# Kernel optimization log

Measured on AMD Instinct MI355X. Metric: run time of the kernel, lower is better.

Reference implementation:

```python
import jax, jax.numpy as jnp
import numpy as np

CHANNELS = 512
GROUPS = 32
EPS = 1e-6


def setup_inputs() -> dict:
    key = jax.random.key(0)
    ks = jax.random.split(key, 10)
    C = CHANNELS
    s = 1.0 / np.sqrt(C)
    return {
        "hidden_states": jax.random.normal(ks[0], (4, 64, 64, C), dtype=jnp.float32),
        "gn_scale": jnp.ones((C,), dtype=jnp.float32),
        "gn_bias": jnp.zeros((C,), dtype=jnp.float32),
        "wq": jax.random.normal(ks[1], (C, C), dtype=jnp.float32) * s,
        "bq": jnp.zeros((C,), dtype=jnp.float32),
        "wk": jax.random.normal(ks[2], (C, C), dtype=jnp.float32) * s,
        "bk": jnp.zeros((C,), dtype=jnp.float32),
        "wv": jax.random.normal(ks[3], (C, C), dtype=jnp.float32) * s,
        "bv": jnp.zeros((C,), dtype=jnp.float32),
        "wo": jax.random.normal(ks[4], (C, C), dtype=jnp.float32) * s,
        "bo": jnp.zeros((C,), dtype=jnp.float32),
    }


def reference(hidden_states, gn_scale, gn_bias, wq, bq, wk, bk, wv, bv, wo, bo):
    B, H, W, C = hidden_states.shape
    residual = hidden_states
    L = H * W
    x = hidden_states.reshape(B, L, C)

    # GroupNorm: stats over (spatial, channels-within-group), per batch per group
    xg = x.reshape(B, L, GROUPS, C // GROUPS)
    mean = jnp.mean(xg, axis=(1, 3), keepdims=True)
    var = jnp.var(xg, axis=(1, 3), keepdims=True)
    xn = ((xg - mean) * jax.lax.rsqrt(var + EPS)).reshape(B, L, C)
    xn = xn * gn_scale + gn_bias

    # QKV projections (heads=1, head_dim=C)
    q = xn @ wq + bq
    k = xn @ wk + bk
    v = xn @ wv + bv

    scale = 1.0 / jnp.sqrt(jnp.asarray(C, dtype=q.dtype))
    scores = jnp.einsum('bld,bsd->bls', q, k) * scale  # [B, L, L]
    attn = jax.nn.softmax(scores, axis=-1)
    out = jnp.einsum('bls,bsd->bld', attn, v)

    out = out @ wo + bo
    return out.reshape(B, H, W, C) + residual
```

## Files before the change

kernel.cpp:

```cpp
#include <hip/hip_runtime.h>
#include <hip/hip_bf16.h>
#include <stdint.h>

#define BATCH 4
#define SEQ   4096
#define CH    512
#define NGRP  32
#define GEPS  1e-6f

typedef short  short8  __attribute__((ext_vector_type(8)));
typedef float  floatx4 __attribute__((ext_vector_type(4)));
typedef long   longx2  __attribute__((ext_vector_type(2)));

static __device__ __forceinline__ short bf16b(float f) {
    __hip_bfloat16 h = __float2bfloat16(f);
    return __builtin_bit_cast(short, h);
}
static __device__ __forceinline__ float bf2f(short s) {
    unsigned u = ((unsigned)(unsigned short)s) << 16;
    return __builtin_bit_cast(float, u);
}
static __device__ __forceinline__ char fp8b(float f) {
    int pk = __builtin_amdgcn_cvt_pk_fp8_f32(f, f, 0, false);
    return (char)(pk & 0xff);
}

static __device__ __forceinline__ void dma16(const void* g, void* l) {
    __builtin_amdgcn_global_load_lds(
        (const __attribute__((address_space(1))) unsigned int*)g,
        (__attribute__((address_space(3))) unsigned int*)l, 16, 0, 0);
}

static __device__ __forceinline__ float rowmax16(float x) {
    int xi = __builtin_bit_cast(int, x);
    x = fmaxf(x, __builtin_bit_cast(float, __builtin_amdgcn_update_dpp(xi, xi, 0x128, 0xf, 0xf, true)));
    xi = __builtin_bit_cast(int, x);
    x = fmaxf(x, __builtin_bit_cast(float, __builtin_amdgcn_update_dpp(xi, xi, 0x124, 0xf, 0xf, true)));
    xi = __builtin_bit_cast(int, x);
    x = fmaxf(x, __builtin_bit_cast(float, __builtin_amdgcn_update_dpp(xi, xi, 0x122, 0xf, 0xf, true)));
    xi = __builtin_bit_cast(int, x);
    x = fmaxf(x, __builtin_bit_cast(float, __builtin_amdgcn_update_dpp(xi, xi, 0x121, 0xf, 0xf, true)));
    return x;
}

__global__ __launch_bounds__(256) void gn_wt_kernel(const float* __restrict__ x,
                                                    float* __restrict__ statsraw,
                                                    const float* __restrict__ w0,
                                                    const float* __restrict__ w1,
                                                    const float* __restrict__ w2,
                                                    const float* __restrict__ w3,
                                                    short* __restrict__ wT) {
    __shared__ float a1[256], a2[256];
    __shared__ float trs[32][33];
    int blk = blockIdx.x;
    int t = threadIdx.x;
    if (blk < 256) {
        size_t row0 = (size_t)blk * 64;
        int qd = t & 127;
        int rh = t >> 7;
        const float* base = x + row0 * 512 + qd * 4;
        float s1 = 0.f, s2 = 0.f;
        #pragma unroll 4
        for (int i = 0; i < 32; ++i) {
            int r = rh + i * 2;
            float4 v = *reinterpret_cast<const float4*>(base + (size_t)r * 512);
            s1 += v.x + v.y + v.z + v.w;
            s2 += v.x * v.x + v.y * v.y + v.z * v.z + v.w * v.w;
        }
        a1[t] = s1; a2[t] = s2;
        __syncthreads();
        if (t < 32) {
            float u1 = 0.f, u2 = 0.f;
            #pragma unroll
            for (int e = 0; e < 4; ++e) {
                u1 += a1[t * 4 + e] + a1[128 + t * 4 + e];
                u2 += a2[t * 4 + e] + a2[128 + t * 4 + e];
            }
            int b = (int)(row0 >> 12);
            atomicAdd(&statsraw[(b * 32 + t) * 2],     u1);
            atomicAdd(&statsraw[(b * 32 + t) * 2 + 1], u2);
        }
    } else {
        int bz = (blk - 256) >> 8;
        int rem = (blk - 256) & 255;
        int n0 = (rem & 15) * 32, k0 = (rem >> 4) * 32;
        const float* w = (bz == 0) ? w0 : (bz == 1) ? w1 : (bz == 2) ? w2 : w3;
        short* out = wT + (size_t)bz * CH * CH;
        int tx = t & 31, ty = t >> 5;
        #pragma unroll
        for (int i = 0; i < 4; ++i) {
            int kk = ty + i * 8;
            trs[kk][tx] = w[(size_t)(k0 + kk) * CH + n0 + tx];
        }
        __syncthreads();
        #pragma unroll
        for (int i = 0; i < 4; ++i) {
            int nn = ty + i * 8;
            out[(size_t)(n0 + nn) * CH + k0 + tx] = bf16b(trs[tx][nn]);
        }
    }
}

__global__ __launch_bounds__(256) void gn_apply_kernel(const float* __restrict__ x,
                                                       const float* __restrict__ statsraw,
                                                       const float* __restrict__ gsc,
                                                       const float* __restrict__ gbs,
                                                       short* __restrict__ xn) {
    int i4 = blockIdx.x * 256 + threadIdx.x;
    int base = i4 * 4;
    int b = base >> 21;
    int c = base & 511;
    int sidx = (b * 32 + (c >> 4)) * 2;
    float s1 = statsraw[sidx], s2 = statsraw[sidx + 1];
    float mean = s1 * (1.f / 65536.f);
    float var  = s2 * (1.f / 65536.f) - mean * mean;
    float rstd = rsqrtf(var + GEPS);
    float4 xv = reinterpret_cast<const float4*>(x)[i4];
    float4 sv = *reinterpret_cast<const float4*>(gsc + c);
    float4 bv = *reinterpret_cast<const float4*>(gbs + c);
    union { short s[4]; uint2 u; } p;
    p.s[0] = bf16b((xv.x - mean) * rstd * sv.x + bv.x);
    p.s[1] = bf16b((xv.y - mean) * rstd * sv.y + bv.y);
    p.s[2] = bf16b((xv.z - mean) * rstd * sv.z + bv.z);
    p.s[3] = bf16b((xv.w - mean) * rstd * sv.w + bv.w);
    reinterpret_cast<uint2*>(xn)[i4] = p.u;
}

__global__ __launch_bounds__(256) void gemm_qkv_kernel(const short* __restrict__ A,
                                                       const short* __restrict__ wT,
                                                       const float* __restrict__ bq,
                                                       const float* __restrict__ bk,
                                                       const float* __restrict__ bv,
                                                       char* __restrict__ q8,
                                                       char* __restrict__ k8,
                                                       char* __restrict__ vT8) {
    __shared__ short As[128 * 64];
    __shared__ short Bs[128 * 64];
    __shared__ char  vls[128 * 144];
    int m0 = blockIdx.x * 128;
    int nblk = blockIdx.y;
    int which = nblk >> 2;
    int n0 = (nblk & 3) * 128;
    const short* BT = wT + (size_t)which * 512 * 512;
    const float* bias = (which == 0) ? bq : (which == 1) ? bk : bv;
    int t = threadIdx.x;
    int w = t >> 6, lane = t & 63;
    int wr = w >> 1, wc = w & 1;
    int l15 = lane & 15, l4 = lane >> 4;
    floatx4 acc[4][4];
    #pragma unroll
    for (int i = 0; i < 4; ++i)
        #pragma unroll
        for (int j = 0; j < 4; ++j) acc[i][j] = (floatx4){0.f, 0.f, 0.f, 0.f};

    for (int k0 = 0; k0 < 512; k0 += 64) {
        __syncthreads();
        #pragma unroll
        for (int i = 0; i < 4; ++i) {
            int c = i * 256 + t;
            int row = c >> 3, j = (c & 7) ^ (row & 7);
            dma16(&A[(size_t)(m0 + row) * 512 + k0 + j * 8], &As[(c & ~63) * 8]);
            dma16(&BT[(size_t)(n0 + row) * 512 + k0 + j * 8], &Bs[(c & ~63) * 8]);
        }
        __syncthreads();
        #pragma unroll
        for (int kk = 0; kk < 64; kk += 32) {
            short8 af[4], bf[4];
            #pragma unroll
            for (int i = 0; i < 4; ++i) {
                int row = wr * 64 + i * 16 + l15;
                int j = (kk >> 3) + l4;
                af[i] = *reinterpret_cast<const short8*>(&As[(row * 8 + (j ^ (l15 & 7))) * 8]);
            }
            #pragma unroll
            for (int j2 = 0; j2 < 4; ++j2) {
                int row = wc * 64 + j2 * 16 + l15;
                int j = (kk >> 3) + l4;
                bf[j2] = *reinterpret_cast<const short8*>(&Bs[(row * 8 + (j ^ (l15 & 7))) * 8]);
            }
            #pragma unroll
            for (int i = 0; i < 4; ++i)
                #pragma unroll
                for (int j2 = 0; j2 < 4; ++j2)
                    acc[i][j2] = __builtin_amdgcn_mfma_f32_16x16x32_bf16(af[i], bf[j2], acc[i][j2], 0, 0, 0);
        }
    }
    if (which == 0) {
        #pragma unroll
        for (int i = 0; i < 4; ++i)
            #pragma unroll
            for (int j = 0; j < 4; ++j)
                #pragma unroll
                for (int r = 0; r < 4; ++r) {
                    int rl = wr * 64 + i * 16 + l4 * 4 + r;
                    int cl = wc * 64 + j * 16 + l15;
                    vls[rl * 144 + cl] = fp8b(acc[i][j][r] + bias[n0 + cl]);
                }
        __syncthreads();
        #pragma unroll
        for (int p = 0; p < 4; ++p) {
            int slot = p * 256 + t;
            int c = slot >> 3, off = (slot & 7) * 16;
            uint4 v;
            __builtin_memcpy(&v, &vls[c * 144 + off], 16);
            *reinterpret_cast<uint4*>(&q8[(size_t)(m0 + c) * 512 + n0 + off]) = v;
        }
    } else if (which == 1) {
        #pragma unroll
        for (int i = 0; i < 4; ++i)
            #pragma unroll
            for (int j = 0; j < 4; ++j)
                #pragma unroll
                for (int r = 0; r < 4; ++r) {
                    int rl = wr * 64 + i * 16 + l4 * 4 + r;
                    int cl = wc * 64 + j * 16 + l15;
                    int sblk = rl >> 5, srow = rl & 15, hp = (rl >> 4) & 1;
                    int ch = (cl >> 3) ^ (srow & 7);
                    vls[sblk * 4096 + srow * 256 + ch * 16 + hp * 8 + (cl & 7)]
                        = fp8b(acc[i][j][r] + bias[n0 + cl]);
                }
        __syncthreads();
        int bb = m0 >> 12, sb0 = (m0 & 4095) >> 5;
        #pragma unroll
        for (int p = 0; p < 4; ++p) {
            int u = p * 256 + t;
            int sblk = u >> 8, srow = (u >> 4) & 15, ch = u & 15;
            uint4 v;
            __builtin_memcpy(&v, &vls[sblk * 4096 + srow * 256 + ((ch ^ (srow & 7)) * 16)], 16);
            char* dst = k8 + (size_t)bb * 2097152 + (size_t)(sb0 + sblk) * 16384
                      + srow * 1024 + n0 * 2 + ch * 16;
            *reinterpret_cast<uint4*>(dst) = v;
        }
    } else {
        __syncthreads();
        #pragma unroll
        for (int i = 0; i < 4; ++i)
            #pragma unroll
            for (int j = 0; j < 4; ++j)
                #pragma unroll
                for (int r = 0; r < 4; ++r) {
                    int rl = wr * 64 + i * 16 + l4 * 4 + r;
                    int rp = (rl & ~31) | (((rl & 15) << 1) | ((rl >> 4) & 1));
                    int cl = wc * 64 + j * 16 + l15;
                    vls[cl * 144 + rp] = fp8b(acc[i][j][r] + bias[n0 + cl]);
                }
        __syncthreads();
        int b = m0 >> 12, l0 = m0 & 4095;
        #pragma unroll
        for (int p = 0; p < 4; ++p) {
            int slot = p * 256 + t;
            int c = slot >> 3, off = (slot & 7) * 16;
            uint4 v;
            __builtin_memcpy(&v, &vls[c * 144 + off], 16);
            int dcol = n0 + c;
            int g = dcol >> 5, rr = dcol & 15, h = (dcol >> 4) & 1;
            int s = l0 + off;
            int sb = s >> 5, mb = (s & 31) >> 3;
            char* dst = vT8 + (size_t)b * 2097152 + (size_t)sb * 16384
                      + (size_t)((((g * 16 + rr) * 4 + mb) * 16) + h * 8);
            unsigned long long lo = ((unsigned long long)v.y << 32) | v.x;
            unsigned long long hi = ((unsigned long long)v.w << 32) | v.z;
            *reinterpret_cast<unsigned long long*>(dst)      = lo;
            *reinterpret_cast<unsigned long long*>(dst + 16) = hi;
        }
    }
}

__global__ __launch_bounds__(256) void gemm_bt_kernel(const short* __restrict__ Opart,
                                                      const float* __restrict__ ml,
                                                      const short* __restrict__ BT,
                                                      const float* __restrict__ bias,
                                                      float* __restrict__ outf,
                                                      const float* __restrict__ resid) {
    __shared__ short As[128 * 64];
    __shared__ short Bs[128 * 64];
    int m0 = blockIdx.x * 128, n0 = blockIdx.y * 128;
    int t = threadIdx.x;
    int w = t >> 6, lane = t & 63;
    int wr = w >> 1, wc = w & 1;
    int l15 = lane & 15, l4 = lane >> 4;
    const size_t PART = (size_t)BATCH * SEQ;
    floatx4 acc[4][4];
    #pragma unroll
    for (int i = 0; i < 4; ++i)
        #pragma unroll
        for (int j = 0; j < 4; ++j) acc[i][j] = (floatx4){0.f, 0.f, 0.f, 0.f};

    float e0h[4], e1h[4];
    #pragma unroll
    for (int i = 0; i < 4; ++i) {
        int rl = (i * 256 + t) >> 3;
        size_t rowg = (size_t)(m0 + rl);
        float mA = ml[rowg * 2],          lA = ml[rowg * 2 + 1];
        float mB = ml[(PART + rowg) * 2], lB = ml[(PART + rowg) * 2 + 1];
        float mm = fmaxf(mA, mB);
        float e0 = exp2f(mA - mm), e1 = exp2f(mB - mm);
        float inv = 1.f / (e0 * lA + e1 * lB);
        e0h[i] = e0 * inv; e1h[i] = e1 * inv;
    }

    for (int k0 = 0; k0 < 512; k0 += 64) {
        __syncthreads();
        #pragma unroll
        for (int i = 0; i < 4; ++i) {
            int c = i * 256 + t;
            int rl = c >> 3, j = (c & 7) ^ (rl & 7);
            size_t rowg = (size_t)(m0 + rl);
            const short* s0 = Opart + rowg * 512 + k0 + j * 8;
            const short* s1 = s0 + PART * 512;
            uint4 a0 = *reinterpret_cast<const uint4*>(s0);
            uint4 a1 = *reinterpret_cast<const uint4*>(s1);
            union { uint4 u; short s[8]; } ua, ub, uo;
            ua.u = a0; ub.u = a1;
            #pragma unroll
            for (int e = 0; e < 8; ++e)
                uo.s[e] = bf16b(bf2f(ua.s[e]) * e0h[i] + bf2f(ub.s[e]) * e1h[i]);
            *reinterpret_cast<uint4*>(&As[c * 8]) = uo.u;
            dma16(&BT[(size_t)(n0 + rl) * 512 + k0 + j * 8], &Bs[(c & ~63) * 8]);
        }
        __syncthreads();
        #pragma unroll
        for (int kk = 0; kk < 64; kk += 32) {
            short8 af[4], bf[4];
            #pragma unroll
            for (int i = 0; i < 4; ++i) {
                int row = wr * 64 + i * 16 + l15;
                int j = (kk >> 3) + l4;
                af[i] = *reinterpret_cast<const short8*>(&As[(row * 8 + (j ^ (l15 & 7))) * 8]);
            }
            #pragma unroll
            for (int j2 = 0; j2 < 4; ++j2) {
                int row = wc * 64 + j2 * 16 + l15;
                int j = (kk >> 3) + l4;
                bf[j2] = *reinterpret_cast<const short8*>(&Bs[(row * 8 + (j ^ (l15 & 7))) * 8]);
            }
            #pragma unroll
            for (int i = 0; i < 4; ++i)
                #pragma unroll
                for (int j2 = 0; j2 < 4; ++j2)
                    acc[i][j2] = __builtin_amdgcn_mfma_f32_16x16x32_bf16(af[i], bf[j2], acc[i][j2], 0, 0, 0);
        }
    }
    #pragma unroll
    for (int i = 0; i < 4; ++i)
        #pragma unroll
        for (int j = 0; j < 4; ++j)
            #pragma unroll
            for (int r = 0; r < 4; ++r) {
                int row = m0 + wr * 64 + i * 16 + l4 * 4 + r;
                int col = n0 + wc * 64 + j * 16 + l15;
                float vv = acc[i][j][r] + bias[col];
                outf[(size_t)row * 512 + col] = vv + resid[(size_t)row * 512 + col];
            }
}

__global__ __launch_bounds__(512, 1) void flash_kernel(const char* __restrict__ q8,
                                                       const char* __restrict__ k8,
                                                       const char* __restrict__ v8,
                                                       short* __restrict__ Opart,
                                                       float* __restrict__ ml) {
    __shared__ __align__(16) char smem[141312];
    int bx = blockIdx.x;
    int pb = bx & 7;
    int part = pb >> 2, b = pb & 3;
    int q0 = (bx >> 3) * 128;
    int t = threadIdx.x, w = t >> 6, lane = t & 63;
    int l15 = lane & 15, l4 = lane >> 4;
    const float c2 = 0.06375873735f;
    const float MARGIN = 7.2134752f;

    long qf[16];
    {
        const char* qrow = q8 + ((size_t)b * SEQ + q0 + w * 16 + l15) * 512;
        #pragma unroll
        for (int ks = 0; ks < 16; ++ks)
            qf[ks] = *reinterpret_cast<const long*>(qrow + ks * 32 + l4 * 8);
    }

    floatx4 acc[32];
    #pragma unroll
    for (int i = 0; i < 32; ++i) acc[i] = (floatx4){0.f, 0.f, 0.f, 0.f};
    floatx4 lacc = (floatx4){0.f, 0.f, 0.f, 0.f};
    float mused[4] = {-1e30f, -1e30f, -1e30f, -1e30f};

    const long ones = 0x3838383838383838L;

    const char* kbase = k8 + (size_t)b * SEQ * 512;
    const char* vbase = v8 + (size_t)b * 512 * SEQ;
    const int sb0 = part * 64;

    const int ksw = l15 & 7;
    const int vsw = (l15 >> 1) & 3;
    const char* kA_E = smem + ((l15 * 64 + (l4 ^ ksw)) << 4);
    const char* kA_O = smem + ((l15 * 64 + ((4 + l4) ^ ksw)) << 4);
    const char* vA   = smem + 65536 + ((l15 * 4 + (l4 ^ vsw)) << 4);
    char* Ps = smem + 131072 + w * 1280;

    int kSrc[4], vSrc[4];
    #pragma unroll
    for (int i = 0; i < 4; ++i) {
        int c = i * 512 + t;
        int tile = c >> 10, cw = c & 1023;
        kSrc[i] = tile * 16384 + (((cw & ~63) | ((cw & 63) ^ ((cw >> 6) & 7))) << 4);
        vSrc[i] = tile * 16384 + (((cw & ~3)  | ((cw & 3)  ^ ((cw >> 3) & 3))) << 4);
    }
    const int ldsD = (t & ~63) << 4;

    auto stage = [&](int sb, int buf) {
        const char* kt = kbase + (size_t)sb * 16384;
        const char* vt = vbase + (size_t)sb * 16384;
        char* Kd = smem + buf * 32768 + ldsD;
        char* Vd = smem + 65536 + buf * 32768 + ldsD;
        #pragma unroll
        for (int i = 0; i < 4; ++i) dma16(kt + kSrc[i], Kd + i * 8192);
        #pragma unroll
        for (int i = 0; i < 4; ++i) dma16(vt + vSrc[i], Vd + i * 8192);
    };

    stage(sb0, 0);
    __syncthreads();

    for (int it = 0; it < 32; ++it) {
        int cur = it & 1;
        int coff = cur << 15;
        if (it + 1 < 32) stage(sb0 + 2 * (it + 1), 1 - cur);

        floatx4 s00 = (floatx4){0.f, 0.f, 0.f, 0.f};
        floatx4 s01 = (floatx4){0.f, 0.f, 0.f, 0.f};
        floatx4 s10 = (floatx4){0.f, 0.f, 0.f, 0.f};
        floatx4 s11 = (floatx4){0.f, 0.f, 0.f, 0.f};
        #pragma unroll
        for (int j = 0; j < 8; ++j) {
            longx2 kE0 = *reinterpret_cast<const longx2*>(kA_E + coff + j * 128);
            longx2 kO0 = *reinterpret_cast<const longx2*>(kA_O + coff + j * 128);
            longx2 kE1 = *reinterpret_cast<const longx2*>(kA_E + coff + 16384 + j * 128);
            longx2 kO1 = *reinterpret_cast<const longx2*>(kA_O + coff + 16384 + j * 128);
            s00 = __builtin_amdgcn_mfma_f32_16x16x32_fp8_fp8(qf[2 * j],     kE0[0], s00, 0, 0, 0);
            s01 = __builtin_amdgcn_mfma_f32_16x16x32_fp8_fp8(qf[2 * j],     kE0[1], s01, 0, 0, 0);
            s10 = __builtin_amdgcn_mfma_f32_16x16x32_fp8_fp8(qf[2 * j],     kE1[0], s10, 0, 0, 0);
            s11 = __builtin_amdgcn_mfma_f32_16x16x32_fp8_fp8(qf[2 * j],     kE1[1], s11, 0, 0, 0);
            s00 = __builtin_amdgcn_mfma_f32_16x16x32_fp8_fp8(qf[2 * j + 1], kO0[0], s00, 0, 0, 0);
            s01 = __builtin_amdgcn_mfma_f32_16x16x32_fp8_fp8(qf[2 * j + 1], kO0[1], s01, 0, 0, 0);
            s10 = __builtin_amdgcn_mfma_f32_16x16x32_fp8_fp8(qf[2 * j + 1], kO1[0], s10, 0, 0, 0);
            s11 = __builtin_amdgcn_mfma_f32_16x16x32_fp8_fp8(qf[2 * j + 1], kO1[1], s11, 0, 0, 0);
        }

        float v00[4], v01[4], v10[4], v11[4], nm4[4];
        bool need = false;
        #pragma unroll
        for (int r = 0; r < 4; ++r) {
            v00[r] = s00[r] * c2; v01[r] = s01[r] * c2;
            v10[r] = s10[r] * c2; v11[r] = s11[r] * c2;
            nm4[r] = rowmax16(fmaxf(fmaxf(v00[r], v01[r]), fmaxf(v10[r], v11[r])));
            need |= (nm4[r] > mused[r] + MARGIN);
        }
        if (__ballot(need)) {
            #pragma unroll
            for (int r = 0; r < 4; ++r) {
                float nm = fmaxf(mused[r], nm4[r]);
                float al = exp2f(mused[r] - nm);
                lacc[r] *= al;
                #pragma unroll
                for (int i = 0; i < 32; ++i) acc[i][r] *= al;
                mused[r] = nm;
            }
        }
        #pragma unroll
        for (int r = 0; r < 4; ++r) {
            int pk0 = __builtin_amdgcn_cvt_pk_fp8_f32(exp2f(v00[r] - mused[r]),
                                                      exp2f(v01[r] - mused[r]), 0, false);
            int pk1 = __builtin_amdgcn_cvt_pk_fp8_f32(exp2f(v10[r] - mused[r]),
                                                      exp2f(v11[r] - mused[r]), 0, false);
            *reinterpret_cast<short*>(Ps + (l4 * 4 + r) * 40 + l15 * 2)       = (short)pk0;
            *reinterpret_cast<short*>(Ps + 640 + (l4 * 4 + r) * 40 + l15 * 2) = (short)pk1;
        }

        long pf0, pf1;
        __builtin_memcpy(&pf0, (const char*)__builtin_assume_aligned(Ps + l15 * 40 + l4 * 8, 8), 8);
        __builtin_memcpy(&pf1, (const char*)__builtin_assume_aligned(Ps + 640 + l15 * 40 + l4 * 8, 8), 8);
        lacc = __builtin_amdgcn_mfma_f32_16x16x32_fp8_fp8(pf0, ones, lacc, 0, 0, 0);
        lacc = __builtin_amdgcn_mfma_f32_16x16x32_fp8_fp8(pf1, ones, lacc, 0, 0, 0);
        #pragma unroll
        for (int g = 0; g < 16; ++g) {
            longx2 va = *reinterpret_cast<const longx2*>(vA + coff + g * 1024);
            acc[2 * g]     = __builtin_amdgcn_mfma_f32_16x16x32_fp8_fp8(pf0, va[0], acc[2 * g],     0, 0, 0);
            acc[2 * g + 1] = __builtin_amdgcn_mfma_f32_16x16x32_fp8_fp8(pf0, va[1], acc[2 * g + 1], 0, 0, 0);
        }
        #pragma unroll
        for (int g = 0; g < 16; ++g) {
            longx2 vb = *reinterpret_cast<const longx2*>(vA + coff + 16384 + g * 1024);
            acc[2 * g]     = __builtin_amdgcn_mfma_f32_16x16x32_fp8_fp8(pf1, vb[0], acc[2 * g],     0, 0, 0);
            acc[2 * g + 1] = __builtin_amdgcn_mfma_f32_16x16x32_fp8_fp8(pf1, vb[1], acc[2 * g + 1], 0, 0, 0);
        }

        __syncthreads();
    }

    short* obase = Opart + (((size_t)part * BATCH + b) * SEQ + q0 + w * 16) * 512;
    #pragma unroll
    for (int r = 0; r < 4; ++r) {
        #pragma unroll
        for (int tt = 0; tt < 32; ++tt)
            obase[(size_t)(l4 * 4 + r) * 512 + tt * 16 + l15] = bf16b(acc[tt][r]);
    }
    if (l15 == 0) {
        #pragma unroll
        for (int r = 0; r < 4; ++r) {
            size_t rowg = ((size_t)part * BATCH + b) * SEQ + q0 + w * 16 + l4 * 4 + r;
            ml[rowg * 2]     = mused[r];
            ml[rowg * 2 + 1] = lacc[r];
        }
    }
}

extern "C" void kernel_launch(void* const* d_in, const int* in_sizes, int n_in,
                              void* d_out, int out_size, void* d_ws, size_t ws_size,
                              hipStream_t stream) {
    const float* x   = (const float*)d_in[0];
    const float* gsc = (const float*)d_in[1];
    const float* gbs = (const float*)d_in[2];
    const float* wq  = (const float*)d_in[3];
    const float* bq  = (const float*)d_in[4];
    const float* wk  = (const float*)d_in[5];
    const float* bk  = (const float*)d_in[6];
    const float* wv  = (const float*)d_in[7];
    const float* bv  = (const float*)d_in[8];
    const float* wo  = (const float*)d_in[9];
    const float* bo  = (const float*)d_in[10];
    float* out = (float*)d_out;

    char* ws = (char*)d_ws;
    const size_t MB = 1ull << 20;
    short* xn    = (short*)ws;
    char*  q8    = (char*)(ws + 16 * MB);
    char*  k8    = (char*)(ws + 24 * MB);
    char*  vT8   = (char*)(ws + 32 * MB);
    short* Opart = (short*)(ws + 40 * MB);
    short* wT    = (short*)(ws + 72 * MB);
    float* stats = (float*)(ws + 74 * MB);
    float* ml    = (float*)(ws + 74 * MB + 65536);

    hipMemsetAsync(stats, 0, 256 * sizeof(float), stream);
    gn_wt_kernel<<<1280, 256, 0, stream>>>(x, stats, wq, wk, wv, wo, wT);
    gn_apply_kernel<<<8192, 256, 0, stream>>>(x, stats, gsc, gbs, xn);

    short* woT = wT + 786432;

    gemm_qkv_kernel<<<dim3(128, 12), 256, 0, stream>>>(xn, wT, bq, bk, bv, q8, k8, vT8);
    flash_kernel<<<256, 512, 0, stream>>>(q8, k8, vT8, Opart, ml);
    gemm_bt_kernel<<<dim3(128, 4), 256, 0, stream>>>(Opart, ml, woT, bo, out, x);
}
```

Measured before the change: 277.6 us.

## Process two 16-row query groups per wave in flash kernel with 4 waves

The flash attention block shrinks from 8 waves to 4, and each wave now handles two 16-row query groups. Each K/V fragment read from LDS therefore feeds two sets of MFMAs, which halves LDS read traffic per unit of compute and improves reuse. The cost is twice the accumulator registers per wave (64 floatx4 for O plus Q fragments). With one block per CU and 4 waves, occupancy and latency hiding drop, and register spilling is a risk.

New measurement: 836.3 us. 201% more time.

```diff
diff --git a/kernel.cpp b/kernel.cpp
--- a/kernel.cpp
+++ b/kernel.cpp
@@ -354,7 +354,7 @@
             }
 }
 
-__global__ __launch_bounds__(512, 1) void flash_kernel(const char* __restrict__ q8,
+__global__ __launch_bounds__(256, 1) void flash_kernel(const char* __restrict__ q8,
                                                        const char* __restrict__ k8,
                                                        const char* __restrict__ v8,
                                                        short* __restrict__ Opart,
@@ -369,19 +369,25 @@
     const float c2 = 0.06375873735f;
     const float MARGIN = 7.2134752f;
 
-    long qf[16];
-    {
-        const char* qrow = q8 + ((size_t)b * SEQ + q0 + w * 16 + l15) * 512;
+    long qf[2][16];
+    #pragma unroll
+    for (int qg = 0; qg < 2; ++qg) {
+        const char* qrow = q8 + ((size_t)b * SEQ + q0 + qg * 64 + w * 16 + l15) * 512;
         #pragma unroll
         for (int ks = 0; ks < 16; ++ks)
-            qf[ks] = *reinterpret_cast<const long*>(qrow + ks * 32 + l4 * 8);
-    }
-
-    floatx4 acc[32];
-    #pragma unroll
-    for (int i = 0; i < 32; ++i) acc[i] = (floatx4){0.f, 0.f, 0.f, 0.f};
-    floatx4 lacc = (floatx4){0.f, 0.f, 0.f, 0.f};
-    float mused[4] = {-1e30f, -1e30f, -1e30f, -1e30f};
+            qf[qg][ks] = *reinterpret_cast<const long*>(qrow + ks * 32 + l4 * 8);
+    }
+
+    floatx4 acc[2][32];
+    #pragma unroll
+    for (int qg = 0; qg < 2; ++qg)
+        #pragma unroll
+        for (int i = 0; i < 32; ++i) acc[qg][i] = (floatx4){0.f, 0.f, 0.f, 0.f};
+    floatx4 lacc[2];
+    lacc[0] = (floatx4){0.f, 0.f, 0.f, 0.f};
+    lacc[1] = (floatx4){0.f, 0.f, 0.f, 0.f};
+    float mused[2][4] = {{-1e30f, -1e30f, -1e30f, -1e30f},
+                         {-1e30f, -1e30f, -1e30f, -1e30f}};
 
     const long ones = 0x3838383838383838L;
 
@@ -394,12 +400,12 @@
     const char* kA_E = smem + ((l15 * 64 + (l4 ^ ksw)) << 4);
     const char* kA_O = smem + ((l15 * 64 + ((4 + l4) ^ ksw)) << 4);
     const char* vA   = smem + 65536 + ((l15 * 4 + (l4 ^ vsw)) << 4);
-    char* Ps = smem + 131072 + w * 1280;
-
-    int kSrc[4], vSrc[4];
-    #pragma unroll
-    for (int i = 0; i < 4; ++i) {
-        int c = i * 512 + t;
+    char* Ps = smem + 131072 + w * 2560;
+
+    int kSrc[8], vSrc[8];
+    #pragma unroll
+    for (int i = 0; i < 8; ++i) {
+        int c = i * 256 + t;
         int tile = c >> 10, cw = c & 1023;
         kSrc[i] = tile * 16384 + (((cw & ~63) | ((cw & 63) ^ ((cw >> 6) & 7))) << 4);
         vSrc[i] = tile * 16384 + (((cw & ~3)  | ((cw & 3)  ^ ((cw >> 3) & 3))) << 4);
@@ -412,9 +418,9 @@
         char* Kd = smem + buf * 32768 + ldsD;
         char* Vd = smem + 65536 + buf * 32768 + ldsD;
         #pragma unroll
-        for (int i = 0; i < 4; ++i) dma16(kt + kSrc[i], Kd + i * 8192);
-        #pragma unroll
-        for (int i = 0; i < 4; ++i) dma16(vt + vSrc[i], Vd + i * 8192);
+        for (int i = 0; i < 8; ++i) dma16(kt + kSrc[i], Kd + i * 4096);
+        #pragma unroll
+        for (int i = 0; i < 8; ++i) dma16(vt + vSrc[i], Vd + i * 4096);
     };
 
     stage(sb0, 0);
@@ -425,90 +431,112 @@
         int coff = cur << 15;
         if (it + 1 < 32) stage(sb0 + 2 * (it + 1), 1 - cur);
 
-        floatx4 s00 = (floatx4){0.f, 0.f, 0.f, 0.f};
-        floatx4 s01 = (floatx4){0.f, 0.f, 0.f, 0.f};
-        floatx4 s10 = (floatx4){0.f, 0.f, 0.f, 0.f};
-        floatx4 s11 = (floatx4){0.f, 0.f, 0.f, 0.f};
+        floatx4 s0[4], s1[4];
+        #pragma unroll
+        for (int i = 0; i < 4; ++i) {
+            s0[i] = (floatx4){0.f, 0.f, 0.f, 0.f};
+            s1[i] = (floatx4){0.f, 0.f, 0.f, 0.f};
+        }
         #pragma unroll
         for (int j = 0; j < 8; ++j) {
             longx2 kE0 = *reinterpret_cast<const longx2*>(kA_E + coff + j * 128);
             longx2 kO0 = *reinterpret_cast<const longx2*>(kA_O + coff + j * 128);
             longx2 kE1 = *reinterpret_cast<const longx2*>(kA_E + coff + 16384 + j * 128);
             longx2 kO1 = *reinterpret_cast<const longx2*>(kA_O + coff + 16384 + j * 128);
-            s00 = __builtin_amdgcn_mfma_f32_16x16x32_fp8_fp8(qf[2 * j],     kE0[0], s00, 0, 0, 0);
-            s01 = __builtin_amdgcn_mfma_f32_16x16x32_fp8_fp8(qf[2 * j],     kE0[1], s01, 0, 0, 0);
-            s10 = __builtin_amdgcn_mfma_f32_16x16x32_fp8_fp8(qf[2 * j],     kE1[0], s10, 0, 0, 0);
-            s11 = __builtin_amdgcn_mfma_f32_16x16x32_fp8_fp8(qf[2 * j],     kE1[1], s11, 0, 0, 0);
-            s00 = __builtin_amdgcn_mfma_f32_16x16x32_fp8_fp8(qf[2 * j + 1], kO0[0], s00, 0, 0, 0);
-            s01 = __builtin_amdgcn_mfma_f32_16x16x32_fp8_fp8(qf[2 * j + 1], kO0[1], s01, 0, 0, 0);
-            s10 = __builtin_amdgcn_mfma_f32_16x16x32_fp8_fp8(qf[2 * j + 1], kO1[0], s10, 0, 0, 0);
-            s11 = __builtin_amdgcn_mfma_f32_16x16x32_fp8_fp8(qf[2 * j + 1], kO1[1], s11, 0, 0, 0);
-        }
-
-        float v00[4], v01[4], v10[4], v11[4], nm4[4];
-        bool need = false;
-        #pragma unroll
-        for (int r = 0; r < 4; ++r) {
-            v00[r] = s00[r] * c2; v01[r] = s01[r] * c2;
-            v10[r] = s10[r] * c2; v11[r] = s11[r] * c2;
-            nm4[r] = rowmax16(fmaxf(fmaxf(v00[r], v01[r]), fmaxf(v10[r], v11[r])));
-            need |= (nm4[r] > mused[r] + MARGIN);
-        }
-        if (__ballot(need)) {
+            s0[0] = __builtin_amdgcn_mfma_f32_16x16x32_fp8_fp8(qf[0][2 * j],     kE0[0], s0[0], 0, 0, 0);
+            s0[1] = __builtin_amdgcn_mfma_f32_16x16x32_fp8_fp8(qf[0][2 * j],     kE0[1], s0[1], 0, 0, 0);
+            s0[2] = __builtin_amdgcn_mfma_f32_16x16x32_fp8_fp8(qf[0][2 * j],     kE1[0], s0[2], 0, 0, 0);
+            s0[3] = __builtin_amdgcn_mfma_f32_16x16x32_fp8_fp8(qf[0][2 * j],     kE1[1], s0[3], 0, 0, 0);
+            s1[0] = __builtin_amdgcn_mfma_f32_16x16x32_fp8_fp8(qf[1][2 * j],     kE0[0], s1[0], 0, 0, 0);
+            s1[1] = __builtin_amdgcn_mfma_f32_16x16x32_fp8_fp8(qf[1][2 * j],     kE0[1], s1[1], 0, 0, 0);
+            s1[2] = __builtin_amdgcn_mfma_f32_16x16x32_fp8_fp8(qf[1][2 * j],     kE1[0], s1[2], 0, 0, 0);
+            s1[3] = __builtin_amdgcn_mfma_f32_16x16x32_fp8_fp8(qf[1][2 * j],     kE1[1], s1[3], 0, 0, 0);
+            s0[0] = __builtin_amdgcn_mfma_f32_16x16x32_fp8_fp8(qf[0][2 * j + 1], kO0[0], s0[0], 0, 0, 0);
+            s0[1] = __builtin_amdgcn_mfma_f32_16x16x32_fp8_fp8(qf[0][2 * j + 1], kO0[1], s0[1], 0, 0, 0);
+            s0[2] = __builtin_amdgcn_mfma_f32_16x16x32_fp8_fp8(qf[0][2 * j + 1], kO1[0], s0[2], 0, 0, 0);
+            s0[3] = __builtin_amdgcn_mfma_f32_16x16x32_fp8_fp8(qf[0][2 * j + 1], kO1[1], s0[3], 0, 0, 0);
+            s1[0] = __builtin_amdgcn_mfma_f32_16x16x32_fp8_fp8(qf[1][2 * j + 1], kO0[0], s1[0], 0, 0, 0);
+            s1[1] = __builtin_amdgcn_mfma_f32_16x16x32_fp8_fp8(qf[1][2 * j + 1], kO0[1], s1[1], 0, 0, 0);
+            s1[2] = __builtin_amdgcn_mfma_f32_16x16x32_fp8_fp8(qf[1][2 * j + 1], kO1[0], s1[2], 0, 0, 0);
+            s1[3] = __builtin_amdgcn_mfma_f32_16x16x32_fp8_fp8(qf[1][2 * j + 1], kO1[1], s1[3], 0, 0, 0);
+        }
+
+        long pf[2][2];
+        #pragma unroll
+        for (int qg = 0; qg < 2; ++qg) {
+            const floatx4* sq = (qg == 0) ? s0 : s1;
+            float v00[4], v01[4], v10[4], v11[4], nm4[4];
+            bool need = false;
             #pragma unroll
             for (int r = 0; r < 4; ++r) {
-                float nm = fmaxf(mused[r], nm4[r]);
-                float al = exp2f(mused[r] - nm);
-                lacc[r] *= al;
+                v00[r] = sq[0][r] * c2; v01[r] = sq[1][r] * c2;
+                v10[r] = sq[2][r] * c2; v11[r] = sq[3][r] * c2;
+                nm4[r] = rowmax16(fmaxf(fmaxf(v00[r], v01[r]), fmaxf(v10[r], v11[r])));
+                need |= (nm4[r] > mused[qg][r] + MARGIN);
+            }
+            if (__ballot(need)) {
                 #pragma unroll
-                for (int i = 0; i < 32; ++i) acc[i][r] *= al;
-                mused[r] = nm;
-            }
-        }
-        #pragma unroll
-        for (int r = 0; r < 4; ++r) {
-            int pk0 = __builtin_amdgcn_cvt_pk_fp8_f32(exp2f(v00[r] - mused[r]),
-                                                      exp2f(v01[r] - mused[r]), 0, false);
-            int pk1 = __builtin_amdgcn_cvt_pk_fp8_f32(exp2f(v10[r] - mused[r]),
-                                                      exp2f(v11[r] - mused[r]), 0, false);
-            *reinterpret_cast<short*>(Ps + (l4 * 4 + r) * 40 + l15 * 2)       = (short)pk0;
-            *reinterpret_cast<short*>(Ps + 640 + (l4 * 4 + r) * 40 + l15 * 2) = (short)pk1;
-        }
-
-        long pf0, pf1;
-        __builtin_memcpy(&pf0, (const char*)__builtin_assume_aligned(Ps + l15 * 40 + l4 * 8, 8), 8);
-        __builtin_memcpy(&pf1, (const char*)__builtin_assume_aligned(Ps + 640 + l15 * 40 + l4 * 8, 8), 8);
-        lacc = __builtin_amdgcn_mfma_f32_16x16x32_fp8_fp8(pf0, ones, lacc, 0, 0, 0);
-        lacc = __builtin_amdgcn_mfma_f32_16x16x32_fp8_fp8(pf1, ones, lacc, 0, 0, 0);
+                for (int r = 0; r < 4; ++r) {
+                    float nm = fmaxf(mused[qg][r], nm4[r]);
+                    float al = exp2f(mused[qg][r] - nm);
+                    lacc[qg][r] *= al;
+                    #pragma unroll
+                    for (int i = 0; i < 32; ++i) acc[qg][i][r] *= al;
+                    mused[qg][r] = nm;
+                }
+            }
+            char* Pq = Ps + qg * 1280;
+            #pragma unroll
+            for (int r = 0; r < 4; ++r) {
+                int pk0 = __builtin_amdgcn_cvt_pk_fp8_f32(exp2f(v00[r] - mused[qg][r]),
+                                                          exp2f(v01[r] - mused[qg][r]), 0, false);
+                int pk1 = __builtin_amdgcn_cvt_pk_fp8_f32(exp2f(v10[r] - mused[qg][r]),
+                                                          exp2f(v11[r] - mused[qg][r]), 0, false);
+                *reinterpret_cast<short*>(Pq + (l4 * 4 + r) * 40 + l15 * 2)       = (short)pk0;
+                *reinterpret_cast<short*>(Pq + 640 + (l4 * 4 + r) * 40 + l15 * 2) = (short)pk1;
+            }
+            __builtin_memcpy(&pf[qg][0], (const char*)__builtin_assume_aligned(Pq + l15 * 40 + l4 * 8, 8), 8);
+            __builtin_memcpy(&pf[qg][1], (const char*)__builtin_assume_aligned(Pq + 640 + l15 * 40 + l4 * 8, 8), 8);
+            lacc[qg] = __builtin_amdgcn_mfma_f32_16x16x32_fp8_fp8(pf[qg][0], ones, lacc[qg], 0, 0, 0);
+            lacc[qg] = __builtin_amdgcn_mfma_f32_16x16x32_fp8_fp8(pf[qg][1], ones, lacc[qg], 0, 0, 0);
+        }
+
         #pragma unroll
         for (int g = 0; g < 16; ++g) {
             longx2 va = *reinterpret_cast<const longx2*>(vA + coff + g * 1024);
-            acc[2 * g]     = __builtin_amdgcn_mfma_f32_16x16x32_fp8_fp8(pf0, va[0], acc[2 * g],     0, 0, 0);
-            acc[2 * g + 1] = __builtin_amdgcn_mfma_f32_16x16x32_fp8_fp8(pf0, va[1], acc[2 * g + 1], 0, 0, 0);
+            acc[0][2 * g]     = __builtin_amdgcn_mfma_f32_16x16x32_fp8_fp8(pf[0][0], va[0], acc[0][2 * g],     0, 0, 0);
+            acc[0][2 * g + 1] = __builtin_amdgcn_mfma_f32_16x16x32_fp8_fp8(pf[0][0], va[1], acc[0][2 * g + 1], 0, 0, 0);
+            acc[1][2 * g]     = __builtin_amdgcn_mfma_f32_16x16x32_fp8_fp8(pf[1][0], va[0], acc[1][2 * g],     0, 0, 0);
+            acc[1][2 * g + 1] = __builtin_amdgcn_mfma_f32_16x16x32_fp8_fp8(pf[1][0], va[1], acc[1][2 * g + 1], 0, 0, 0);
         }
         #pragma unroll
         for (int g = 0; g < 16; ++g) {
             longx2 vb = *reinterpret_cast<const longx2*>(vA + coff + 16384 + g * 1024);
-            acc[2 * g]     = __builtin_amdgcn_mfma_f32_16x16x32_fp8_fp8(pf1, vb[0], acc[2 * g],     0, 0, 0);
-            acc[2 * g + 1] = __builtin_amdgcn_mfma_f32_16x16x32_fp8_fp8(pf1, vb[1], acc[2 * g + 1], 0, 0, 0);
-        }
-
-        __syncthreads();
-    }
-
-    short* obase = Opart + (((size_t)part * BATCH + b) * SEQ + q0 + w * 16) * 512;
-    #pragma unroll
-    for (int r = 0; r < 4; ++r) {
-        #pragma unroll
-        for (int tt = 0; tt < 32; ++tt)
-            obase[(size_t)(l4 * 4 + r) * 512 + tt * 16 + l15] = bf16b(acc[tt][r]);
-    }
-    if (l15 == 0) {
+            acc[0][2 * g]     = __builtin_amdgcn_mfma_f32_16x16x32_fp8_fp8(pf[0][1], vb[0], acc[0][2 * g],     0, 0, 0);
+            acc[0][2 * g + 1] = __builtin_amdgcn_mfma_f32_16x16x32_fp8_fp8(pf[0][1], vb[1], acc[0][2 * g + 1], 0, 0, 0);
+            acc[1][2 * g]     = __builtin_amdgcn_mfma_f32_16x16x32_fp8_fp8(pf[1][1], vb[0], acc[1][2 * g],     0, 0, 0);
+            acc[1][2 * g + 1] = __builtin_amdgcn_mfma_f32_16x16x32_fp8_fp8(pf[1][1], vb[1], acc[1][2 * g + 1], 0, 0, 0);
+        }
+
+        __syncthreads();
+    }
+
+    #pragma unroll
+    for (int qg = 0; qg < 2; ++qg) {
+        short* obase = Opart + (((size_t)part * BATCH + b) * SEQ + q0 + qg * 64 + w * 16) * 512;
         #pragma unroll
         for (int r = 0; r < 4; ++r) {
-            size_t rowg = ((size_t)part * BATCH + b) * SEQ + q0 + w * 16 + l4 * 4 + r;
-            ml[rowg * 2]     = mused[r];
-            ml[rowg * 2 + 1] = lacc[r];
+            #pragma unroll
+            for (int tt = 0; tt < 32; ++tt)
+                obase[(size_t)(l4 * 4 + r) * 512 + tt * 16 + l15] = bf16b(acc[qg][tt][r]);
+        }
+        if (l15 == 0) {
+            #pragma unroll
+            for (int r = 0; r < 4; ++r) {
+                size_t rowg = ((size_t)part * BATCH + b) * SEQ + q0 + qg * 64 + w * 16 + l4 * 4 + r;
+                ml[rowg * 2]     = mused[qg][r];
+                ml[rowg * 2 + 1] = lacc[qg][r];
+            }
         }
     }
 }
@@ -547,6 +575,6 @@
     short* woT = wT + 786432;
 
     gemm_qkv_kernel<<<dim3(128, 12), 256, 0, stream>>>(xn, wT, bq, bk, bv, q8, k8, vT8);
-    flash_kernel<<<256, 512, 0, stream>>>(q8, k8, vT8, Opart, ml);
+    flash_kernel<<<256, 256, 0, stream>>>(q8, k8, vT8, Opart, ml);
     gemm_bt_kernel<<<dim3(128, 4), 256, 0, stream>>>(Opart, ml, woT, bo, out, x);
 }
```
